# Optimization experiments

Hardware: AMD Instinct MI355X
Metric: run time of the kernel (lower is better)

## Reference

```python
import jax, jax.numpy as jnp
import numpy as np
from jax import lax


def conv2d(x, w, b=None, stride=1, pad=0):
    y = lax.conv_general_dilated(x, w, (stride, stride), [(pad, pad), (pad, pad)],
                                 dimension_numbers=('NCHW', 'OIHW', 'NCHW'))
    if b is not None:
        y = y + b[None, :, None, None]
    return y


def bilinear_resize_ac(S, Ho, Wo):
    # F.interpolate(..., mode='bilinear', align_corners=True)
    B, C, H, W = S.shape
    ys = jnp.linspace(0.0, H - 1.0, Ho)
    xs = jnp.linspace(0.0, W - 1.0, Wo)
    y0 = jnp.floor(ys).astype(jnp.int32); y1 = jnp.minimum(y0 + 1, H - 1); wy = ys - y0
    x0 = jnp.floor(xs).astype(jnp.int32); x1 = jnp.minimum(x0 + 1, W - 1); wx = xs - x0
    Sy = S[:, :, y0, :] * (1 - wy)[None, None, :, None] + S[:, :, y1, :] * wy[None, None, :, None]
    return Sy[:, :, :, x0] * (1 - wx)[None, None, None, :] + Sy[:, :, :, x1] * wx[None, None, None, :]


def deform_conv(x, offset, weight, bias=None, mask=None, stride=1, pad=1, dil=1):
    # (Modulated) deformable conv, deformable_groups=1; DCNv2 semantics:
    # offset channels are (dy, dx) pairs per kernel tap; zero padding outside.
    B, C, H, W = x.shape
    O, Ci, kh, kw = weight.shape
    K = kh * kw
    Ho, Wo = offset.shape[2], offset.shape[3]
    off = offset.reshape(B, K, 2, Ho, Wo)
    kyy, kxx = jnp.meshgrid(jnp.arange(kh) * dil, jnp.arange(kw) * dil, indexing='ij')
    kyy = kyy.reshape(K).astype(x.dtype); kxx = kxx.reshape(K).astype(x.dtype)
    base_y = (jnp.arange(Ho) * stride - pad).astype(x.dtype)
    base_x = (jnp.arange(Wo) * stride - pad).astype(x.dtype)
    py = base_y[None, None, :, None] + kyy[None, :, None, None] + off[:, :, 0]  # [B,K,Ho,Wo]
    px = base_x[None, None, None, :] + kxx[None, :, None, None] + off[:, :, 1]
    y0 = jnp.floor(py); x0 = jnp.floor(px)
    dy = py - y0; dx = px - x0
    y0i = y0.astype(jnp.int32); x0i = x0.astype(jnp.int32)
    xf = x.reshape(B, C, H * W)

    def corner(yi, xi, w):
        valid = (yi >= 0) & (yi <= H - 1) & (xi >= 0) & (xi <= W - 1)
        yc = jnp.clip(yi, 0, H - 1); xc = jnp.clip(xi, 0, W - 1)
        idx = (yc * W + xc).reshape(B, -1)  # [B, K*Ho*Wo]
        g = jax.vmap(lambda f, i: f[:, i])(xf, idx)  # [B, C, K*Ho*Wo]
        g = g.reshape(B, C, K, Ho, Wo)
        return g * (w * valid.astype(x.dtype))[:, None]

    s = (corner(y0i, x0i, (1 - dy) * (1 - dx))
         + corner(y0i, x0i + 1, (1 - dy) * dx)
         + corner(y0i + 1, x0i, dy * (1 - dx))
         + corner(y0i + 1, x0i + 1, dy * dx))  # [B,C,K,Ho,Wo]
    if mask is not None:
        s = s * mask[:, None]  # [B,1,K,Ho,Wo]
    out = jnp.einsum('bckhw,ock->bohw', s, weight.reshape(O, Ci, K))
    if bias is not None:
        out = out + bias[None, :, None, None]
    return out


def setup_inputs():
    key = jax.random.key(0)
    ks = jax.random.split(key, 16)
    B, Cin, Cout, H, W = 8, 256, 256, 64, 64

    def n(k, shape, s):
        return jax.random.normal(k, shape, jnp.float32) * s

    return {
        'x': jax.random.normal(ks[0], (B, Cin, H, W), jnp.float32),
        'S': jax.random.normal(ks[1], (B, 3, 128, 128), jnp.float32),
        'sp_w1': n(ks[2], (64, 3, 3, 3), 0.2), 'sp_b1': jnp.zeros(64), 'sp_s1': jnp.ones(64) + n(ks[3], (64,), 0.05), 'sp_o1': n(ks[3], (64,), 0.05),
        'sp_w2': n(ks[4], (64, 64, 3, 3), 0.05), 'sp_b2': jnp.zeros(64), 'sp_s2': jnp.ones(64) + n(ks[5], (64,), 0.05), 'sp_o2': n(ks[5], (64,), 0.05),
        'sp_w3': n(ks[6], (64, 64, 3, 3), 0.05), 'sp_b3': jnp.zeros(64), 'sp_s3': jnp.ones(64) + n(ks[7], (64,), 0.05), 'sp_o3': n(ks[7], (64,), 0.05),
        'off_w': n(ks[8], (18, 64, 3, 3), 0.05), 'off_b': jnp.zeros(18),
        'dc_off_w': n(ks[9], (18, 64, 3, 3), 0.05), 'dc_off_b': jnp.zeros(18),
        'dc_w': n(ks[10], (64, 64, 3, 3), 0.04),
        'm_w': n(ks[11], (9, 64, 1, 1), 0.1), 'm_b': jnp.zeros(9),
        'weight': n(ks[12], (Cout, Cin, 3, 3), 0.02), 'bias': jnp.zeros(Cout),
    }


def reference(x, S, sp_w1, sp_b1, sp_s1, sp_o1, sp_w2, sp_b2, sp_s2, sp_o2,
              sp_w3, sp_b3, sp_s3, sp_o3, off_w, off_b, dc_off_w, dc_off_b,
              dc_w, m_w, m_b, weight, bias):
    H, W = x.shape[2], x.shape[3]
    Si = bilinear_resize_ac(S, H, W)
    h = jax.nn.relu(conv2d(Si, sp_w1, sp_b1, 1, 1) * sp_s1[None, :, None, None] + sp_o1[None, :, None, None])
    h = jax.nn.relu(conv2d(h, sp_w2, sp_b2, 1, 1) * sp_s2[None, :, None, None] + sp_o2[None, :, None, None])
    h = jax.nn.relu(conv2d(h, sp_w3, sp_b3, 1, 1) * sp_s3[None, :, None, None] + sp_o3[None, :, None, None])
    offset = conv2d(h, off_w, off_b, 1, 1)                 # [B,18,H,W]
    dc_off = conv2d(h, dc_off_w, dc_off_b, 1, 1)           # internal offsets of weight_generator1 (DCNv1)
    feat = deform_conv(h, dc_off, dc_w, None, None, 1, 1, 1)
    mask = jax.nn.sigmoid(conv2d(feat, m_w, m_b, 1, 0))    # [B,9,H,W]
    return deform_conv(x, offset, weight, bias, mask, 1, 1, 1)
```

## Files before the change

kernel.cpp:

```cpp
#include <hip/hip_runtime.h>
#include <hip/hip_bf16.h>

typedef unsigned short u16;
typedef unsigned int u32;
typedef __attribute__((ext_vector_type(8))) short short8;
typedef __attribute__((ext_vector_type(4))) unsigned short ush4;
typedef __attribute__((ext_vector_type(16))) float f32x16;

#define OXT   0
#define OSI   (OXT + 8388608)
#define OA    (OSI + 98304)
#define OB    (OA + 2097152)
#define OC    (OB + 2097152)
#define OOFFS (OC + 2097152)
#define OMSK  (OOFFS + 1179648)
#define OWT   (OMSK + 294912)
#define OWSP1 (OWT + 589824)
#define OBSP1 (OWSP1 + 1728)
#define OWSP2 (OBSP1 + 64)
#define OBSP2 (OWSP2 + 36864)
#define OWSP3 (OBSP2 + 64)
#define OBSP3 (OWSP3 + 36864)
#define OWOFF (OBSP3 + 64)
#define OBOFF (OWOFF + 36864)
#define OWDC  (OBOFF + 64)

__device__ __forceinline__ u16 f2bf(float f) {
    __hip_bfloat16 hb = __float2bfloat16(f);
    return __builtin_bit_cast(u16, hb);
}
__device__ __forceinline__ float bf2f(u16 v) {
    return __builtin_bit_cast(float, (u32)v << 16);
}
__device__ __forceinline__ int sswz(int kg, int px) {
    return (px & ~7) | ((px ^ kg) & 7);
}

__global__ __launch_bounds__(256) void prep_k(
    const float* __restrict__ weight,
    const float* __restrict__ sp_w1, const float* __restrict__ sp_s1,
    const float* __restrict__ sp_w2, const float* __restrict__ sp_s2,
    const float* __restrict__ sp_w3, const float* __restrict__ sp_s3,
    const float* __restrict__ off_w, const float* __restrict__ dc_off_w,
    const float* __restrict__ dc_w,
    const float* __restrict__ sp_b1, const float* __restrict__ sp_o1,
    const float* __restrict__ sp_b2, const float* __restrict__ sp_o2,
    const float* __restrict__ sp_b3, const float* __restrict__ sp_o3,
    const float* __restrict__ off_b, const float* __restrict__ dc_off_b,
    float* __restrict__ ws)
{
    int i = blockIdx.x * 256 + threadIdx.x;
    if (i < 589824) {
        int j = i & 7; int o = (i >> 3) & 255; int kg = i >> 11;
        int K = kg * 8 + j; int k = K >> 8; int c = K & 255;
        ((u16*)(ws + OWT))[i] = f2bf(weight[o * 2304 + c * 9 + k]);
        return;
    }
    i -= 589824;
    if (i < 1728) {
        int o = i & 63; int kc = i >> 6; int c = kc % 3; int k = kc / 3;
        ws[OWSP1 + i] = sp_w1[(o * 3 + c) * 9 + k] * sp_s1[o];
        return;
    }
    i -= 1728;
    if (i < 36864) {
        int e = i & 7; int o = (i >> 3) & 63; int kg = (i >> 9) & 7; int tp = i >> 12;
        ((u16*)(ws + OWSP2))[i] = f2bf(sp_w2[(o * 64 + kg * 8 + e) * 9 + tp] * sp_s2[o]);
        return;
    }
    i -= 36864;
    if (i < 36864) {
        int e = i & 7; int o = (i >> 3) & 63; int kg = (i >> 9) & 7; int tp = i >> 12;
        ((u16*)(ws + OWSP3))[i] = f2bf(sp_w3[(o * 64 + kg * 8 + e) * 9 + tp] * sp_s3[o]);
        return;
    }
    i -= 36864;
    if (i < 36864) {
        int e = i & 7; int o = (i >> 3) & 63; int kg = (i >> 9) & 7; int tp = i >> 12;
        int c = kg * 8 + e;
        float v = 0.f;
        if (o < 18) v = off_w[(o * 64 + c) * 9 + tp];
        else if (o < 36) v = dc_off_w[((o - 18) * 64 + c) * 9 + tp];
        ((u16*)(ws + OWOFF))[i] = f2bf(v);
        return;
    }
    i -= 36864;
    if (i < 36864) {
        int e = i & 7; int o = (i >> 3) & 63; int kg = (i >> 9) & 7; int tp = i >> 12;
        ((u16*)(ws + OWDC))[i] = f2bf(dc_w[(o * 64 + kg * 8 + e) * 9 + tp]);
        return;
    }
    i -= 36864;
    if (i < 64) { ws[OBSP1 + i] = sp_b1[i] * sp_s1[i] + sp_o1[i]; return; }
    i -= 64;
    if (i < 64) { ws[OBSP2 + i] = sp_b2[i] * sp_s2[i] + sp_o2[i]; return; }
    i -= 64;
    if (i < 64) { ws[OBSP3 + i] = sp_b3[i] * sp_s3[i] + sp_o3[i]; return; }
    i -= 64;
    if (i < 64) { ws[OBOFF + i] = (i < 18) ? off_b[i] : (i < 36 ? dc_off_b[i - 18] : 0.f); return; }
}

__global__ __launch_bounds__(256) void transpose_x_k(const float* __restrict__ x,
                                                     u16* __restrict__ xT)
{
    __shared__ float tile[64][65];
    int blk = blockIdx.x;
    int chunk = blk & 3; int by = blk >> 2;
    int b = by >> 6; int y = by & 63;
    int c0 = chunk * 64;
    int t = threadIdx.x;
    for (int i = t; i < 4096; i += 256) {
        int ci = i >> 6, xi = i & 63;
        tile[ci][xi] = x[((b * 256 + c0 + ci) * 64 + y) * 64 + xi];
    }
    __syncthreads();
    for (int i = t; i < 4096; i += 256) {
        int xi = i >> 6, ci = i & 63;
        xT[((b * 64 + y) * 64 + xi) * 256 + c0 + ci] = f2bf(tile[ci][xi]);
    }
}

__global__ __launch_bounds__(256) void resize_k(const float* __restrict__ S,
                                                float* __restrict__ Si)
{
    int i = blockIdx.x * 256 + threadIdx.x;
    if (i >= 8 * 64 * 64 * 3) return;
    int c = i % 3; int x = (i / 3) & 63; int y = (i / 192) & 63; int b = i / 12288;
    const float sc = 127.0f / 63.0f;
    float sy = y * sc, sx = x * sc;
    float fy = floorf(sy), fx = floorf(sx);
    int y0 = (int)fy, x0 = (int)fx;
    int y1 = min(y0 + 1, 127), x1 = min(x0 + 1, 127);
    float wy = sy - fy, wx = sx - fx;
    const float* Sb = S + (size_t)(b * 3 + c) * 16384;
    float v00 = Sb[y0 * 128 + x0], v01 = Sb[y0 * 128 + x1];
    float v10 = Sb[y1 * 128 + x0], v11 = Sb[y1 * 128 + x1];
    Si[i] = (v00 * (1.f - wy) + v10 * wy) * (1.f - wx)
          + (v01 * (1.f - wy) + v11 * wy) * wx;
}

__global__ __launch_bounds__(256) void conv_in_k(const float* __restrict__ in,
                                                 const float* __restrict__ wt,
                                                 const float* __restrict__ bias,
                                                 u16* __restrict__ out)
{
    __shared__ float rows[3][66][3];
    int by = blockIdx.x; int b = by >> 6; int y = by & 63;
    int t = threadIdx.x;
    for (int i = t; i < 3 * 66 * 3; i += 256) {
        int r = i / 198; int rem = i - r * 198;
        int xi = rem / 3; int c = rem - xi * 3;
        int yy = y - 1 + r, xx = xi - 1;
        float v = 0.f;
        if (yy >= 0 && yy < 64 && xx >= 0 && xx < 64)
            v = in[(((b * 64 + yy) * 64 + xx) * 3) + c];
        rows[r][xi][c] = v;
    }
    __syncthreads();
    int o4 = (t & 15) * 4; int xg = t >> 4;
    float acc[4][4];
    #pragma unroll
    for (int oi = 0; oi < 4; oi++) {
        float bv = bias[o4 + oi];
        #pragma unroll
        for (int xi = 0; xi < 4; xi++) acc[oi][xi] = bv;
    }
    for (int k = 0; k < 9; k++) {
        int dy = k / 3, dx = k - 3 * (k / 3);
        for (int c = 0; c < 3; c++) {
            float4 w = *reinterpret_cast<const float4*>(&wt[(k * 3 + c) * 64 + o4]);
            #pragma unroll
            for (int xi = 0; xi < 4; xi++) {
                float iv = rows[dy][xg * 4 + xi + dx][c];
                acc[0][xi] = fmaf(w.x, iv, acc[0][xi]);
                acc[1][xi] = fmaf(w.y, iv, acc[1][xi]);
                acc[2][xi] = fmaf(w.z, iv, acc[2][xi]);
                acc[3][xi] = fmaf(w.w, iv, acc[3][xi]);
            }
        }
    }
    #pragma unroll
    for (int xi = 0; xi < 4; xi++) {
        int x = xg * 4 + xi;
        ush4 v;
        v.x = f2bf(fmaxf(acc[0][xi], 0.f));
        v.y = f2bf(fmaxf(acc[1][xi], 0.f));
        v.z = f2bf(fmaxf(acc[2][xi], 0.f));
        v.w = f2bf(fmaxf(acc[3][xi], 0.f));
        *reinterpret_cast<ush4*>(&out[((size_t)(by * 64 + x)) * 64 + o4]) = v;
    }
}

template <int MODE, bool RELU>
__global__ __launch_bounds__(256) void conv_mfma_k(const u16* __restrict__ in,
                                                   const u16* __restrict__ wm,
                                                   const float* __restrict__ bias,
                                                   u16* __restrict__ outH,
                                                   float* __restrict__ outF)
{
    __shared__ __attribute__((aligned(16))) char lds_h[3 * 66 * 128];
    __shared__ __attribute__((aligned(16))) u16 wtap[2][8][64][8];

    int t = threadIdx.x;
    int b = blockIdx.x >> 6; int y = blockIdx.x & 63;
    int pix0 = b * 4096 + y * 64;
    int wid = t >> 6, lane = t & 63;
    int lrow = lane & 31, lhi = lane >> 5;
    int o0 = (wid & 1) << 5;
    int px0 = (wid >> 1) << 5;
    int px = px0 + lrow;

    for (int i = t; i < 3 * 66 * 8; i += 256) {
        int r = i / 528; int rem = i - r * 528;
        int xi = rem >> 3; int g = rem & 7;
        int yy = y - 1 + r, xx = xi - 1;
        short8 v = {0,0,0,0,0,0,0,0};
        if (yy >= 0 && yy < 64 && xx >= 0 && xx < 64)
            v = *reinterpret_cast<const short8*>(&in[(size_t)((b * 4096 + yy * 64 + xx)) * 64 + g * 8]);
        int byte = (r * 66 + xi) * 128 + ((g * 16) ^ ((xi & 7) << 4));
        *reinterpret_cast<short8*>(lds_h + byte) = v;
    }
    {
        const char* gb = (const char*)(wm);
        char* lb = (char*)&wtap[0][0][0][0];
        #pragma unroll
        for (int i = 0; i < 2; i++) {
            int off = i * 4096 + wid * 1024;
            __builtin_amdgcn_global_load_lds(
                (const __attribute__((address_space(1))) void*)(gb + off + lane * 16),
                (__attribute__((address_space(3))) void*)(lb + off), 16, 0, 0);
        }
    }
    __syncthreads();

    f32x16 acc;
    #pragma unroll
    for (int r = 0; r < 16; r++) acc[r] = 0.f;

    #pragma unroll
    for (int tap = 0; tap < 9; tap++) {
        int cur = tap & 1, nxt = cur ^ 1;
        if (tap < 8) {
            const char* gb = (const char*)(wm + (size_t)(tap + 1) * 4096);
            char* lb = (char*)&wtap[nxt][0][0][0];
            #pragma unroll
            for (int i = 0; i < 2; i++) {
                int off = i * 4096 + wid * 1024;
                __builtin_amdgcn_global_load_lds(
                    (const __attribute__((address_space(1))) void*)(gb + off + lane * 16),
                    (__attribute__((address_space(3))) void*)(lb + off), 16, 0, 0);
            }
        }
        int dy = tap / 3, dx = tap - 3 * (tap / 3);
        int xi = px + dx;
        int rowbyte = (dy * 66 + xi) * 128;
        int swz = (xi & 7) << 4;
        #pragma unroll
        for (int ks = 0; ks < 4; ks++) {
            int kg = ks * 2 + lhi;
            short8 a0 = *reinterpret_cast<const short8*>(&wtap[cur][kg][o0 + lrow][0]);
            short8 b0 = *reinterpret_cast<const short8*>(lds_h + rowbyte + ((kg * 16) ^ swz));
            acc = __builtin_amdgcn_mfma_f32_32x32x16_bf16(a0, b0, acc, 0, 0, 0);
        }
        if (tap < 8) asm volatile("s_waitcnt vmcnt(0)" ::: "memory");
        __builtin_amdgcn_s_barrier();
    }
    __syncthreads();

    if (MODE == 0) {
        #pragma unroll
        for (int q = 0; q < 4; q++) {
            int ob = o0 + q * 8 + 4 * lhi;
            #pragma unroll
            for (int h = 0; h < 2; h++) {
                float v0 = acc[q * 4 + h * 2] + bias[ob + h * 2];
                float v1 = acc[q * 4 + h * 2 + 1] + bias[ob + h * 2 + 1];
                if (RELU) { v0 = fmaxf(v0, 0.f); v1 = fmaxf(v1, 0.f); }
                u32 pk = (u32)f2bf(v0) | ((u32)f2bf(v1) << 16);
                int byte = px * 128 + (((ob + h * 2) * 2) ^ ((px & 7) << 4));
                *reinterpret_cast<u32*>(lds_h + byte) = pk;
            }
        }
        __syncthreads();
        #pragma unroll
        for (int i = 0; i < 2; i++) {
            int cid = i * 256 + t;
            int p = cid >> 3, g = cid & 7;
            short8 v = *reinterpret_cast<const short8*>(lds_h + p * 128 + ((g * 16) ^ ((p & 7) << 4)));
            *reinterpret_cast<short8*>(&outH[(size_t)(pix0 + p) * 64 + g * 8]) = v;
        }
    } else {
        float* ltf = (float*)lds_h;
        #pragma unroll
        for (int r = 0; r < 16; r++) {
            int o = o0 + (r & 3) + ((r >> 2) << 3) + (lhi << 2);
            if (o < 36) ltf[px * 40 + o] = acc[r] + bias[o];
        }
        __syncthreads();
        for (int i = t; i < 576; i += 256) {
            int p = i / 9, q = i - 9 * (i / 9);
            float4 v = *reinterpret_cast<const float4*>(&ltf[p * 40 + q * 4]);
            *reinterpret_cast<float4*>(&outF[(size_t)(pix0 + p) * 36 + q * 4]) = v;
        }
    }
}

__global__ __launch_bounds__(512) void dconv_small_mfma(
    const u16* __restrict__ h, const float* __restrict__ offs,
    const u16* __restrict__ wdc, const float* __restrict__ m_w,
    const float* __restrict__ m_b, float* __restrict__ maskb)
{
    __shared__ __attribute__((aligned(16))) char smem[49152];
    u16 (*wtile)[8][64][8]  = (u16 (*)[8][64][8])smem;
    u16 (*stile)[8][128][8] = (u16 (*)[8][128][8])(smem + 16384);

    int t = threadIdx.x;
    int id = blockIdx.x;
    int blk = (id & 7) * 32 + (id >> 3);
    int pix0 = blk * 128;
    int b = pix0 >> 12;
    int wid = t >> 6, lane = t & 63;
    int lrow = lane & 31, lhi = lane >> 5;
    int o0 = (wid & 1) << 5;
    int px0 = (wid >> 1) << 5;
    int gp = t >> 2, gsub = t & 3;

    {
        const char* gb = (const char*)wdc;
        char* lb = (char*)&wtile[0][0][0][0];
        __builtin_amdgcn_global_load_lds(
            (const __attribute__((address_space(1))) void*)(gb + wid * 1024 + lane * 16),
            (__attribute__((address_space(3))) void*)(lb + wid * 1024), 16, 0, 0);
    }

    f32x16 acc;
    #pragma unroll
    for (int r = 0; r < 16; r++) acc[r] = 0.f;

    int car[4]; float cwr[4];

    for (int tap = 0; tap < 9; ++tap) {
        int cur = tap & 1, nxt = cur ^ 1;
        {
            int pix = pix0 + gp; int pib = pix & 4095;
            int y = pib >> 6, x = pib & 63;
            float offy = offs[(size_t)pix * 36 + 18 + tap * 2];
            float offx = offs[(size_t)pix * 36 + 18 + tap * 2 + 1];
            float py = (float)(y - 1 + tap / 3) + offy;
            float pxf = (float)(x - 1 + (tap % 3)) + offx;
            float fy = floorf(py), fx = floorf(pxf);
            int y0 = (int)fy, x0 = (int)fx;
            float dyf = py - fy, dxf = pxf - fx;
            #pragma unroll
            for (int j = 0; j < 4; j++) {
                float wj = ((j >> 1) ? dyf : 1.f - dyf) * ((j & 1) ? dxf : 1.f - dxf);
                int yy = y0 + (j >> 1), xx = x0 + (j & 1);
                bool valid = (yy >= 0 && yy < 64 && xx >= 0 && xx < 64);
                int yc = min(max(yy, 0), 63), xc = min(max(xx, 0), 63);
                car[j] = (b * 4096 + yc * 64 + xc) << 6;
                cwr[j] = valid ? wj : 0.f;
            }
        }
        int c = gsub << 4;
        float va[16];
        #pragma unroll
        for (int e = 0; e < 16; e++) va[e] = 0.f;
        #pragma unroll
        for (int j = 0; j < 4; j++) {
            float w = cwr[j];
            const u16* p = h + car[j] + c;
            short8 r0 = *reinterpret_cast<const short8*>(p);
            short8 r1 = *reinterpret_cast<const short8*>(p + 8);
            #pragma unroll
            for (int e = 0; e < 8; e++) {
                va[e]     = fmaf(w, bf2f((u16)r0[e]), va[e]);
                va[8 + e] = fmaf(w, bf2f((u16)r1[e]), va[8 + e]);
            }
        }
        short8 s0, s1;
        #pragma unroll
        for (int e = 0; e < 8; e++) { s0[e] = (short)f2bf(va[e]); s1[e] = (short)f2bf(va[8 + e]); }
        int kg0 = gsub * 2, kg1 = gsub * 2 + 1;
        *reinterpret_cast<short8*>(&stile[cur][kg0][sswz(kg0, gp)][0]) = s0;
        *reinterpret_cast<short8*>(&stile[cur][kg1][sswz(kg1, gp)][0]) = s1;

        asm volatile("s_waitcnt vmcnt(0) lgkmcnt(0)" ::: "memory");
        __builtin_amdgcn_s_barrier();

        #pragma unroll
        for (int ks = 0; ks < 4; ks++) {
            int kg = ks * 2 + lhi;
            short8 a0 = *reinterpret_cast<const short8*>(&wtile[cur][kg][o0 + lrow][0]);
            short8 b0 = *reinterpret_cast<const short8*>(&stile[cur][kg][sswz(kg, px0 + lrow)][0]);
            acc = __builtin_amdgcn_mfma_f32_32x32x16_bf16(a0, b0, acc, 0, 0, 0);
        }
        if (tap < 8) {
            const char* gb = (const char*)(wdc + (size_t)(tap + 1) * 4096);
            char* lb = (char*)&wtile[nxt][0][0][0];
            __builtin_amdgcn_global_load_lds(
                (const __attribute__((address_space(1))) void*)(gb + wid * 1024 + lane * 16),
                (__attribute__((address_space(3))) void*)(lb + wid * 1024), 16, 0, 0);
        }
    }

    __syncthreads();
    float* featl = (float*)smem;
    int pxl = px0 + lrow;
    #pragma unroll
    for (int r = 0; r < 16; r++) {
        int o = o0 + (r & 3) + ((r >> 2) << 3) + (lhi << 2);
        featl[pxl * 65 + o] = acc[r];
    }
    __syncthreads();
    if (t < 256) {
        int p = t >> 1, hh = t & 1;
        int pix = pix0 + p;
        const float* fr = &featl[p * 65];
        int j0 = hh ? 4 : 0, j1 = hh ? 9 : 4;
        for (int j = j0; j < j1; j++) {
            float a = m_b[j];
            #pragma unroll 8
            for (int cc = 0; cc < 64; cc++) a = fmaf(fr[cc], m_w[j * 64 + cc], a);
            maskb[(size_t)pix * 9 + j] = 1.f / (1.f + expf(-a));
        }
    }
}

__global__ __launch_bounds__(512) void dconv_big_mfma(
    const u16* __restrict__ xT, const float* __restrict__ offs,
    const float* __restrict__ maskb, const u16* __restrict__ wKg,
    const float* __restrict__ bias, float* __restrict__ out)
{
    __shared__ __attribute__((aligned(16))) u16 wtile[2][8][256][8];
    __shared__ __attribute__((aligned(16))) u16 stile[2][8][64][8];

    int t = threadIdx.x;
    int id = blockIdx.x;
    int blk = (id & 7) * 64 + (id >> 3);
    int pix0 = blk * 64;
    int b = pix0 >> 12, pib0 = pix0 & 4095;
    int wid = t >> 6, lane = t & 63;
    int lrow = lane & 31, lhi = lane >> 5;
    int o0 = wid << 5;
    int gp = t >> 3, gsub = t & 7;

    {
        const char* gb = (const char*)wKg;
        char* lb = (char*)&wtile[0][0][0][0];
        #pragma unroll
        for (int i = 0; i < 4; i++) {
            int off = i * 8192 + wid * 1024;
            __builtin_amdgcn_global_load_lds(
                (const __attribute__((address_space(1))) void*)(gb + off + lane * 16),
                (__attribute__((address_space(3))) void*)(lb + off), 16, 0, 0);
        }
    }

    f32x16 acc[2];
    #pragma unroll
    for (int fp = 0; fp < 2; fp++)
        #pragma unroll
        for (int r = 0; r < 16; r++) acc[fp][r] = 0.f;

    int car[4]; float cwr[4];

    for (int kt = 0; kt < 36; ++kt) {
        int cur = kt & 1, nxt = cur ^ 1;
        int tap = kt >> 2, chunk = kt & 3;

        if (chunk == 0) {
            int pix = pix0 + gp; int pib = pix & 4095;
            int y = pib >> 6, x = pib & 63;
            float offy = offs[(size_t)pix * 36 + tap * 2];
            float offx = offs[(size_t)pix * 36 + tap * 2 + 1];
            float m = maskb[(size_t)pix * 9 + tap];
            float py = (float)(y - 1 + tap / 3) + offy;
            float pxf = (float)(x - 1 + (tap % 3)) + offx;
            float fy = floorf(py), fx = floorf(pxf);
            int y0 = (int)fy, x0 = (int)fx;
            float dyf = py - fy, dxf = pxf - fx;
            #pragma unroll
            for (int j = 0; j < 4; j++) {
                float wj = ((j >> 1) ? dyf : 1.f - dyf) * ((j & 1) ? dxf : 1.f - dxf);
                int yy = y0 + (j >> 1), xx = x0 + (j & 1);
                bool valid = (yy >= 0 && yy < 64 && xx >= 0 && xx < 64);
                int yc = min(max(yy, 0), 63), xc = min(max(xx, 0), 63);
                car[j] = (b * 4096 + yc * 64 + xc) << 8;
                cwr[j] = valid ? wj * m : 0.f;
            }
        }

        int c = (chunk << 6) + (gsub << 3);
        float va[8];
        #pragma unroll
        for (int e = 0; e < 8; e++) va[e] = 0.f;
        #pragma unroll
        for (int j = 0; j < 4; j++) {
            float w = cwr[j];
            short8 r0 = *reinterpret_cast<const short8*>(xT + car[j] + c);
            #pragma unroll
            for (int e = 0; e < 8; e++) va[e] = fmaf(w, bf2f((u16)r0[e]), va[e]);
        }
        short8 s0;
        #pragma unroll
        for (int e = 0; e < 8; e++) s0[e] = (short)f2bf(va[e]);
        *reinterpret_cast<short8*>(&stile[cur][gsub][sswz(gsub, gp)][0]) = s0;

        asm volatile("s_waitcnt vmcnt(0) lgkmcnt(0)" ::: "memory");
        __builtin_amdgcn_s_barrier();

        #pragma unroll
        for (int ks = 0; ks < 4; ks++) {
            int kg = ks * 2 + lhi;
            short8 a0 = *reinterpret_cast<const short8*>(&wtile[cur][kg][o0 + lrow][0]);
            short8 b0 = *reinterpret_cast<const short8*>(&stile[cur][kg][sswz(kg, lrow)][0]);
            short8 b1 = *reinterpret_cast<const short8*>(&stile[cur][kg][sswz(kg, 32 + lrow)][0]);
            acc[0] = __builtin_amdgcn_mfma_f32_32x32x16_bf16(a0, b0, acc[0], 0, 0, 0);
            acc[1] = __builtin_amdgcn_mfma_f32_32x32x16_bf16(a0, b1, acc[1], 0, 0, 0);
        }
        if (kt < 35) {
            const char* gb = (const char*)(wKg + (size_t)(kt + 1) * 16384);
            char* lb = (char*)&wtile[nxt][0][0][0];
            #pragma unroll
            for (int i = 0; i < 4; i++) {
                int off = i * 8192 + wid * 1024;
                __builtin_amdgcn_global_load_lds(
                    (const __attribute__((address_space(1))) void*)(gb + off + lane * 16),
                    (__attribute__((address_space(3))) void*)(lb + off), 16, 0, 0);
            }
        }
    }

    #pragma unroll
    for (int fp = 0; fp < 2; fp++) {
        #pragma unroll
        for (int r = 0; r < 16; r++) {
            int o = o0 + (r & 3) + ((r >> 2) << 3) + (lhi << 2);
            size_t rowoff = ((size_t)(b * 256 + o) << 12) + pib0;
            out[rowoff + fp * 32 + lrow] = acc[fp][r] + bias[o];
        }
    }
}

extern "C" void kernel_launch(void* const* d_in, const int* in_sizes, int n_in,
                              void* d_out, int out_size, void* d_ws, size_t ws_size,
                              hipStream_t stream)
{
    const float* x        = (const float*)d_in[0];
    const float* S        = (const float*)d_in[1];
    const float* sp_w1    = (const float*)d_in[2];
    const float* sp_b1    = (const float*)d_in[3];
    const float* sp_s1    = (const float*)d_in[4];
    const float* sp_o1    = (const float*)d_in[5];
    const float* sp_w2    = (const float*)d_in[6];
    const float* sp_b2    = (const float*)d_in[7];
    const float* sp_s2    = (const float*)d_in[8];
    const float* sp_o2    = (const float*)d_in[9];
    const float* sp_w3    = (const float*)d_in[10];
    const float* sp_b3    = (const float*)d_in[11];
    const float* sp_s3    = (const float*)d_in[12];
    const float* sp_o3    = (const float*)d_in[13];
    const float* off_w    = (const float*)d_in[14];
    const float* off_b    = (const float*)d_in[15];
    const float* dc_off_w = (const float*)d_in[16];
    const float* dc_off_b = (const float*)d_in[17];
    const float* dc_w     = (const float*)d_in[18];
    const float* m_w      = (const float*)d_in[19];
    const float* m_b      = (const float*)d_in[20];
    const float* weight   = (const float*)d_in[21];
    const float* bias     = (const float*)d_in[22];
    float* out = (float*)d_out;
    float* ws  = (float*)d_ws;

    u16*   xTb   = (u16*)(ws + OXT);
    float* Si    = ws + OSI;
    u16*   h1    = (u16*)(ws + OA);
    u16*   h2    = (u16*)(ws + OB);
    u16*   h3    = (u16*)(ws + OC);
    float* offsb = ws + OOFFS;
    float* maskb = ws + OMSK;

    prep_k<<<2888, 256, 0, stream>>>(weight, sp_w1, sp_s1, sp_w2, sp_s2, sp_w3, sp_s3,
                                     off_w, dc_off_w, dc_w,
                                     sp_b1, sp_o1, sp_b2, sp_o2, sp_b3, sp_o3,
                                     off_b, dc_off_b, ws);
    transpose_x_k<<<2048, 256, 0, stream>>>(x, xTb);
    resize_k<<<384, 256, 0, stream>>>(S, Si);
    conv_in_k<<<512, 256, 0, stream>>>(Si, ws + OWSP1, ws + OBSP1, h1);
    conv_mfma_k<0, true><<<512, 256, 0, stream>>>(h1, (const u16*)(ws + OWSP2),
                                                  ws + OBSP2, h2, nullptr);
    conv_mfma_k<0, true><<<512, 256, 0, stream>>>(h2, (const u16*)(ws + OWSP3),
                                                  ws + OBSP3, h3, nullptr);
    conv_mfma_k<1, false><<<512, 256, 0, stream>>>(h3, (const u16*)(ws + OWOFF),
                                                   ws + OBOFF, nullptr, offsb);
    dconv_small_mfma<<<256, 512, 0, stream>>>(h3, offsb, (const u16*)(ws + OWDC),
                                              m_w, m_b, maskb);
    dconv_big_mfma<<<512, 512, 0, stream>>>(xTb, offsb, maskb,
                                            (const u16*)(ws + OWT), bias, out);
}
```

Before: 147.5 us.

## Enlarge dconv_big pixel tile to 128 and prefetch bilinear gathers one step ahead

The final deformable conv kernel now handles 128 pixels per block instead of 64. Each wave computes a 64x64 output tile with four MFMA accumulators, so every weight tile streamed through LDS is reused across twice as many pixels, and the grid shrinks from 512 to 256 blocks. The corner gathers from xT for the next K-chunk are issued into registers before the barrier and waited with a partial vmcnt, so gather latency overlaps the current MFMA work. The cost is higher register pressure (8 short8 prefetch registers plus 64 accumulator floats), twice the stile LDS, and half as many blocks, which may underfill the 256 CUs.

```diff
diff --git a/kernel.cpp b/kernel.cpp
--- a/kernel.cpp
+++ b/kernel.cpp
@@ -36,6 +36,32 @@
     return (px & ~7) | ((px ^ kg) & 7);
 }
 
+__device__ __forceinline__ void corner_tab_big(
+    int tap, int pix0, int b, int gp,
+    const float* __restrict__ offs, const float* __restrict__ maskb,
+    int* car, float* cwr)
+{
+    int pix = pix0 + gp; int pib = pix & 4095;
+    int y = pib >> 6, x = pib & 63;
+    float offy = offs[(size_t)pix * 36 + tap * 2];
+    float offx = offs[(size_t)pix * 36 + tap * 2 + 1];
+    float m = maskb[(size_t)pix * 9 + tap];
+    float py = (float)(y - 1 + tap / 3) + offy;
+    float pxf = (float)(x - 1 + (tap % 3)) + offx;
+    float fy = floorf(py), fx = floorf(pxf);
+    int y0 = (int)fy, x0 = (int)fx;
+    float dyf = py - fy, dxf = pxf - fx;
+    #pragma unroll
+    for (int j = 0; j < 4; j++) {
+        float wj = ((j >> 1) ? dyf : 1.f - dyf) * ((j & 1) ? dxf : 1.f - dxf);
+        int yy = y0 + (j >> 1), xx = x0 + (j & 1);
+        bool valid = (yy >= 0 && yy < 64 && xx >= 0 && xx < 64);
+        int yc = min(max(yy, 0), 63), xc = min(max(xx, 0), 63);
+        car[j] = (b * 4096 + yc * 64 + xc) << 8;
+        cwr[j] = valid ? wj * m : 0.f;
+    }
+}
+
 __global__ __launch_bounds__(256) void prep_k(
     const float* __restrict__ weight,
     const float* __restrict__ sp_w1, const float* __restrict__ sp_s1,
@@ -432,18 +458,32 @@
     const float* __restrict__ bias, float* __restrict__ out)
 {
     __shared__ __attribute__((aligned(16))) u16 wtile[2][8][256][8];
-    __shared__ __attribute__((aligned(16))) u16 stile[2][8][64][8];
+    __shared__ __attribute__((aligned(16))) u16 stile[2][8][128][8];
 
     int t = threadIdx.x;
     int id = blockIdx.x;
-    int blk = (id & 7) * 64 + (id >> 3);
-    int pix0 = blk * 64;
+    int blk = (id & 7) * 32 + (id >> 3);
+    int pix0 = blk * 128;
     int b = pix0 >> 12, pib0 = pix0 & 4095;
     int wid = t >> 6, lane = t & 63;
     int lrow = lane & 31, lhi = lane >> 5;
-    int o0 = wid << 5;
-    int gp = t >> 3, gsub = t & 7;
-
+    int o0 = (wid & 3) << 6;
+    int px0 = (wid >> 2) << 6;
+    int gp = t >> 2, gsub = t & 3;
+
+    int car[4]; float cwr[4];
+    short8 g[8];
+
+    corner_tab_big(0, pix0, b, gp, offs, maskb, car, cwr);
+    {
+        int c = gsub << 4;
+        #pragma unroll
+        for (int j = 0; j < 4; j++) {
+            const u16* p = xT + car[j] + c;
+            g[j * 2]     = *reinterpret_cast<const short8*>(p);
+            g[j * 2 + 1] = *reinterpret_cast<const short8*>(p + 8);
+        }
+    }
     {
         const char* gb = (const char*)wKg;
         char* lb = (char*)&wtile[0][0][0][0];
@@ -456,67 +496,63 @@
         }
     }
 
-    f32x16 acc[2];
-    #pragma unroll
-    for (int fp = 0; fp < 2; fp++)
-        #pragma unroll
-        for (int r = 0; r < 16; r++) acc[fp][r] = 0.f;
-
-    int car[4]; float cwr[4];
+    f32x16 acc[2][2];
+    #pragma unroll
+    for (int ao = 0; ao < 2; ao++)
+        #pragma unroll
+        for (int bp = 0; bp < 2; bp++)
+            #pragma unroll
+            for (int r = 0; r < 16; r++) acc[ao][bp][r] = 0.f;
 
     for (int kt = 0; kt < 36; ++kt) {
         int cur = kt & 1, nxt = cur ^ 1;
-        int tap = kt >> 2, chunk = kt & 3;
-
-        if (chunk == 0) {
-            int pix = pix0 + gp; int pib = pix & 4095;
-            int y = pib >> 6, x = pib & 63;
-            float offy = offs[(size_t)pix * 36 + tap * 2];
-            float offx = offs[(size_t)pix * 36 + tap * 2 + 1];
-            float m = maskb[(size_t)pix * 9 + tap];
-            float py = (float)(y - 1 + tap / 3) + offy;
-            float pxf = (float)(x - 1 + (tap % 3)) + offx;
-            float fy = floorf(py), fx = floorf(pxf);
-            int y0 = (int)fy, x0 = (int)fx;
-            float dyf = py - fy, dxf = pxf - fx;
-            #pragma unroll
-            for (int j = 0; j < 4; j++) {
-                float wj = ((j >> 1) ? dyf : 1.f - dyf) * ((j & 1) ? dxf : 1.f - dxf);
-                int yy = y0 + (j >> 1), xx = x0 + (j & 1);
-                bool valid = (yy >= 0 && yy < 64 && xx >= 0 && xx < 64);
-                int yc = min(max(yy, 0), 63), xc = min(max(xx, 0), 63);
-                car[j] = (b * 4096 + yc * 64 + xc) << 8;
-                cwr[j] = valid ? wj * m : 0.f;
-            }
-        }
-
-        int c = (chunk << 6) + (gsub << 3);
-        float va[8];
-        #pragma unroll
-        for (int e = 0; e < 8; e++) va[e] = 0.f;
+
+        float va[16];
+        #pragma unroll
+        for (int e = 0; e < 16; e++) va[e] = 0.f;
         #pragma unroll
         for (int j = 0; j < 4; j++) {
             float w = cwr[j];
-            short8 r0 = *reinterpret_cast<const short8*>(xT + car[j] + c);
-            #pragma unroll
-            for (int e = 0; e < 8; e++) va[e] = fmaf(w, bf2f((u16)r0[e]), va[e]);
-        }
-        short8 s0;
-        #pragma unroll
-        for (int e = 0; e < 8; e++) s0[e] = (short)f2bf(va[e]);
-        *reinterpret_cast<short8*>(&stile[cur][gsub][sswz(gsub, gp)][0]) = s0;
-
-        asm volatile("s_waitcnt vmcnt(0) lgkmcnt(0)" ::: "memory");
+            #pragma unroll
+            for (int e = 0; e < 8; e++) {
+                va[e]     = fmaf(w, bf2f((u16)g[j * 2][e]), va[e]);
+                va[8 + e] = fmaf(w, bf2f((u16)g[j * 2 + 1][e]), va[8 + e]);
+            }
+        }
+        short8 s0, s1;
+        #pragma unroll
+        for (int e = 0; e < 8; e++) { s0[e] = (short)f2bf(va[e]); s1[e] = (short)f2bf(va[8 + e]); }
+        int kg0 = gsub * 2, kg1 = gsub * 2 + 1;
+        *reinterpret_cast<short8*>(&stile[cur][kg0][sswz(kg0, gp)][0]) = s0;
+        *reinterpret_cast<short8*>(&stile[cur][kg1][sswz(kg1, gp)][0]) = s1;
+
+        if (kt < 35) {
+            if (((kt + 1) & 3) == 0)
+                corner_tab_big((kt + 1) >> 2, pix0, b, gp, offs, maskb, car, cwr);
+            int c = (((kt + 1) & 3) << 6) + (gsub << 4);
+            #pragma unroll
+            for (int j = 0; j < 4; j++) {
+                const u16* p = xT + car[j] + c;
+                g[j * 2]     = *reinterpret_cast<const short8*>(p);
+                g[j * 2 + 1] = *reinterpret_cast<const short8*>(p + 8);
+            }
+            asm volatile("s_waitcnt vmcnt(8) lgkmcnt(0)" ::: "memory");
+        } else {
+            asm volatile("s_waitcnt vmcnt(0) lgkmcnt(0)" ::: "memory");
+        }
         __builtin_amdgcn_s_barrier();
 
         #pragma unroll
         for (int ks = 0; ks < 4; ks++) {
             int kg = ks * 2 + lhi;
             short8 a0 = *reinterpret_cast<const short8*>(&wtile[cur][kg][o0 + lrow][0]);
-            short8 b0 = *reinterpret_cast<const short8*>(&stile[cur][kg][sswz(kg, lrow)][0]);
-            short8 b1 = *reinterpret_cast<const short8*>(&stile[cur][kg][sswz(kg, 32 + lrow)][0]);
-            acc[0] = __builtin_amdgcn_mfma_f32_32x32x16_bf16(a0, b0, acc[0], 0, 0, 0);
-            acc[1] = __builtin_amdgcn_mfma_f32_32x32x16_bf16(a0, b1, acc[1], 0, 0, 0);
+            short8 a1 = *reinterpret_cast<const short8*>(&wtile[cur][kg][o0 + 32 + lrow][0]);
+            short8 b0 = *reinterpret_cast<const short8*>(&stile[cur][kg][sswz(kg, px0 + lrow)][0]);
+            short8 b1 = *reinterpret_cast<const short8*>(&stile[cur][kg][sswz(kg, px0 + 32 + lrow)][0]);
+            acc[0][0] = __builtin_amdgcn_mfma_f32_32x32x16_bf16(a0, b0, acc[0][0], 0, 0, 0);
+            acc[0][1] = __builtin_amdgcn_mfma_f32_32x32x16_bf16(a0, b1, acc[0][1], 0, 0, 0);
+            acc[1][0] = __builtin_amdgcn_mfma_f32_32x32x16_bf16(a1, b0, acc[1][0], 0, 0, 0);
+            acc[1][1] = __builtin_amdgcn_mfma_f32_32x32x16_bf16(a1, b1, acc[1][1], 0, 0, 0);
         }
         if (kt < 35) {
             const char* gb = (const char*)(wKg + (size_t)(kt + 1) * 16384);
@@ -532,12 +568,14 @@
     }
 
     #pragma unroll
-    for (int fp = 0; fp < 2; fp++) {
+    for (int ao = 0; ao < 2; ao++) {
         #pragma unroll
         for (int r = 0; r < 16; r++) {
-            int o = o0 + (r & 3) + ((r >> 2) << 3) + (lhi << 2);
-            size_t rowoff = ((size_t)(b * 256 + o) << 12) + pib0;
-            out[rowoff + fp * 32 + lrow] = acc[fp][r] + bias[o];
+            int o = o0 + ao * 32 + (r & 3) + ((r >> 2) << 3) + (lhi << 2);
+            float bv = bias[o];
+            size_t rowoff = ((size_t)(b * 256 + o) << 12) + pib0 + px0;
+            out[rowoff + lrow] = acc[ao][0][r] + bv;
+            out[rowoff + 32 + lrow] = acc[ao][1][r] + bv;
         }
     }
 }
@@ -595,6 +633,6 @@
                                                    ws + OBOFF, nullptr, offsb);
     dconv_small_mfma<<<256, 512, 0, stream>>>(h3, offsb, (const u16*)(ws + OWDC),
                                               m_w, m_b, maskb);
-    dconv_big_mfma<<<512, 512, 0, stream>>>(xTb, offsb, maskb,
+    dconv_big_mfma<<<256, 512, 0, stream>>>(xTb, offsb, maskb,
                                             (const u16*)(ws + OWT), bias, out);
 }
```

Result: faster. 137.1 us (-7.1%).

## Software-pipeline deform gather and load weights directly into registers

Applied to the files above, without the earlier changes.

The big deformable conv kernel drops the LDS weight tile and has each wave load its MFMA A fragments straight from global memory into registers. The wave-to-tile mapping changes to 64 output channels by 32 pixels. The bilinear gather for the next K-chunk is issued one iteration ahead, so its global loads overlap the current MFMAs, and the barrier only waits on LDS. This aims to hide gather latency and cut LDS traffic and vmcnt stalls, at the cost of more registers (launch bounds 512,4) and repeated weight reads from L2.

```diff
diff --git a/kernel.cpp b/kernel.cpp
--- a/kernel.cpp
+++ b/kernel.cpp
@@ -34,6 +34,32 @@
 }
 __device__ __forceinline__ int sswz(int kg, int px) {
     return (px & ~7) | ((px ^ kg) & 7);
+}
+
+__device__ __forceinline__ void corner_tab_big(
+    int tap, int pix0, int b, int gp,
+    const float* __restrict__ offs, const float* __restrict__ maskb,
+    int* car, float* cwr)
+{
+    int pix = pix0 + gp; int pib = pix & 4095;
+    int y = pib >> 6, x = pib & 63;
+    float offy = offs[(size_t)pix * 36 + tap * 2];
+    float offx = offs[(size_t)pix * 36 + tap * 2 + 1];
+    float m = maskb[(size_t)pix * 9 + tap];
+    float py = (float)(y - 1 + tap / 3) + offy;
+    float pxf = (float)(x - 1 + (tap % 3)) + offx;
+    float fy = floorf(py), fx = floorf(pxf);
+    int y0 = (int)fy, x0 = (int)fx;
+    float dyf = py - fy, dxf = pxf - fx;
+    #pragma unroll
+    for (int j = 0; j < 4; j++) {
+        float wj = ((j >> 1) ? dyf : 1.f - dyf) * ((j & 1) ? dxf : 1.f - dxf);
+        int yy = y0 + (j >> 1), xx = x0 + (j & 1);
+        bool valid = (yy >= 0 && yy < 64 && xx >= 0 && xx < 64);
+        int yc = min(max(yy, 0), 63), xc = min(max(xx, 0), 63);
+        car[j] = (b * 4096 + yc * 64 + xc) << 8;
+        cwr[j] = valid ? wj * m : 0.f;
+    }
 }
 
 __global__ __launch_bounds__(256) void prep_k(
@@ -426,12 +452,11 @@
     }
 }
 
-__global__ __launch_bounds__(512) void dconv_big_mfma(
+__global__ __launch_bounds__(512, 4) void dconv_big_mfma(
     const u16* __restrict__ xT, const float* __restrict__ offs,
     const float* __restrict__ maskb, const u16* __restrict__ wKg,
     const float* __restrict__ bias, float* __restrict__ out)
 {
-    __shared__ __attribute__((aligned(16))) u16 wtile[2][8][256][8];
     __shared__ __attribute__((aligned(16))) u16 stile[2][8][64][8];
 
     int t = threadIdx.x;
@@ -441,103 +466,114 @@
     int b = pix0 >> 12, pib0 = pix0 & 4095;
     int wid = t >> 6, lane = t & 63;
     int lrow = lane & 31, lhi = lane >> 5;
-    int o0 = wid << 5;
+    int o0 = (wid & 3) << 6;
+    int px0 = (wid >> 2) << 5;
     int gp = t >> 3, gsub = t & 7;
 
+    int car[4]; float cwr[4];
+    short8 g[4];
+    short8 a[8];
+
+    corner_tab_big(0, pix0, b, gp, offs, maskb, car, cwr);
     {
-        const char* gb = (const char*)wKg;
-        char* lb = (char*)&wtile[0][0][0][0];
-        #pragma unroll
-        for (int i = 0; i < 4; i++) {
-            int off = i * 8192 + wid * 1024;
-            __builtin_amdgcn_global_load_lds(
-                (const __attribute__((address_space(1))) void*)(gb + off + lane * 16),
-                (__attribute__((address_space(3))) void*)(lb + off), 16, 0, 0);
-        }
-    }
+        int c = gsub << 3;
+        #pragma unroll
+        for (int j = 0; j < 4; j++)
+            g[j] = *reinterpret_cast<const short8*>(xT + car[j] + c);
+    }
+    {
+        #pragma unroll
+        for (int ks = 0; ks < 4; ks++) {
+            int kgg = ks * 2 + lhi;
+            const u16* base = wKg + ((size_t)kgg * 256 + o0 + lrow) * 8;
+            a[ks]     = *reinterpret_cast<const short8*>(base);
+            a[4 + ks] = *reinterpret_cast<const short8*>(base + 256);
+        }
+    }
+    {
+        float va[8];
+        #pragma unroll
+        for (int e = 0; e < 8; e++) va[e] = 0.f;
+        #pragma unroll
+        for (int j = 0; j < 4; j++) {
+            float w = cwr[j];
+            #pragma unroll
+            for (int e = 0; e < 8; e++) va[e] = fmaf(w, bf2f((u16)g[j][e]), va[e]);
+        }
+        short8 s0;
+        #pragma unroll
+        for (int e = 0; e < 8; e++) s0[e] = (short)f2bf(va[e]);
+        *reinterpret_cast<short8*>(&stile[0][gsub][sswz(gsub, gp)][0]) = s0;
+    }
+    {
+        int c = 64 + (gsub << 3);
+        #pragma unroll
+        for (int j = 0; j < 4; j++)
+            g[j] = *reinterpret_cast<const short8*>(xT + car[j] + c);
+    }
+    asm volatile("s_waitcnt lgkmcnt(0)" ::: "memory");
+    __builtin_amdgcn_s_barrier();
 
     f32x16 acc[2];
     #pragma unroll
-    for (int fp = 0; fp < 2; fp++)
-        #pragma unroll
-        for (int r = 0; r < 16; r++) acc[fp][r] = 0.f;
-
-    int car[4]; float cwr[4];
+    for (int ao = 0; ao < 2; ao++)
+        #pragma unroll
+        for (int r = 0; r < 16; r++) acc[ao][r] = 0.f;
 
     for (int kt = 0; kt < 36; ++kt) {
         int cur = kt & 1, nxt = cur ^ 1;
-        int tap = kt >> 2, chunk = kt & 3;
-
-        if (chunk == 0) {
-            int pix = pix0 + gp; int pib = pix & 4095;
-            int y = pib >> 6, x = pib & 63;
-            float offy = offs[(size_t)pix * 36 + tap * 2];
-            float offx = offs[(size_t)pix * 36 + tap * 2 + 1];
-            float m = maskb[(size_t)pix * 9 + tap];
-            float py = (float)(y - 1 + tap / 3) + offy;
-            float pxf = (float)(x - 1 + (tap % 3)) + offx;
-            float fy = floorf(py), fx = floorf(pxf);
-            int y0 = (int)fy, x0 = (int)fx;
-            float dyf = py - fy, dxf = pxf - fx;
-            #pragma unroll
-            for (int j = 0; j < 4; j++) {
-                float wj = ((j >> 1) ? dyf : 1.f - dyf) * ((j & 1) ? dxf : 1.f - dxf);
-                int yy = y0 + (j >> 1), xx = x0 + (j & 1);
-                bool valid = (yy >= 0 && yy < 64 && xx >= 0 && xx < 64);
-                int yc = min(max(yy, 0), 63), xc = min(max(xx, 0), 63);
-                car[j] = (b * 4096 + yc * 64 + xc) << 8;
-                cwr[j] = valid ? wj * m : 0.f;
-            }
-        }
-
-        int c = (chunk << 6) + (gsub << 3);
-        float va[8];
-        #pragma unroll
-        for (int e = 0; e < 8; e++) va[e] = 0.f;
-        #pragma unroll
-        for (int j = 0; j < 4; j++) {
-            float w = cwr[j];
-            short8 r0 = *reinterpret_cast<const short8*>(xT + car[j] + c);
-            #pragma unroll
-            for (int e = 0; e < 8; e++) va[e] = fmaf(w, bf2f((u16)r0[e]), va[e]);
-        }
-        short8 s0;
-        #pragma unroll
-        for (int e = 0; e < 8; e++) s0[e] = (short)f2bf(va[e]);
-        *reinterpret_cast<short8*>(&stile[cur][gsub][sswz(gsub, gp)][0]) = s0;
-
-        asm volatile("s_waitcnt vmcnt(0) lgkmcnt(0)" ::: "memory");
-        __builtin_amdgcn_s_barrier();
 
         #pragma unroll
         for (int ks = 0; ks < 4; ks++) {
             int kg = ks * 2 + lhi;
-            short8 a0 = *reinterpret_cast<const short8*>(&wtile[cur][kg][o0 + lrow][0]);
-            short8 b0 = *reinterpret_cast<const short8*>(&stile[cur][kg][sswz(kg, lrow)][0]);
-            short8 b1 = *reinterpret_cast<const short8*>(&stile[cur][kg][sswz(kg, 32 + lrow)][0]);
-            acc[0] = __builtin_amdgcn_mfma_f32_32x32x16_bf16(a0, b0, acc[0], 0, 0, 0);
-            acc[1] = __builtin_amdgcn_mfma_f32_32x32x16_bf16(a0, b1, acc[1], 0, 0, 0);
-        }
+            short8 bf = *reinterpret_cast<const short8*>(&stile[cur][kg][sswz(kg, px0 + lrow)][0]);
+            acc[0] = __builtin_amdgcn_mfma_f32_32x32x16_bf16(a[ks], bf, acc[0], 0, 0, 0);
+            acc[1] = __builtin_amdgcn_mfma_f32_32x32x16_bf16(a[4 + ks], bf, acc[1], 0, 0, 0);
+        }
+
         if (kt < 35) {
-            const char* gb = (const char*)(wKg + (size_t)(kt + 1) * 16384);
-            char* lb = (char*)&wtile[nxt][0][0][0];
             #pragma unroll
-            for (int i = 0; i < 4; i++) {
-                int off = i * 8192 + wid * 1024;
-                __builtin_amdgcn_global_load_lds(
-                    (const __attribute__((address_space(1))) void*)(gb + off + lane * 16),
-                    (__attribute__((address_space(3))) void*)(lb + off), 16, 0, 0);
-            }
-        }
-    }
-
-    #pragma unroll
-    for (int fp = 0; fp < 2; fp++) {
+            for (int ks = 0; ks < 4; ks++) {
+                int kgg = (kt + 1) * 8 + ks * 2 + lhi;
+                const u16* base = wKg + ((size_t)kgg * 256 + o0 + lrow) * 8;
+                a[ks]     = *reinterpret_cast<const short8*>(base);
+                a[4 + ks] = *reinterpret_cast<const short8*>(base + 256);
+            }
+            {
+                float va[8];
+                #pragma unroll
+                for (int e = 0; e < 8; e++) va[e] = 0.f;
+                #pragma unroll
+                for (int j = 0; j < 4; j++) {
+                    float w = cwr[j];
+                    #pragma unroll
+                    for (int e = 0; e < 8; e++) va[e] = fmaf(w, bf2f((u16)g[j][e]), va[e]);
+                }
+                short8 s0;
+                #pragma unroll
+                for (int e = 0; e < 8; e++) s0[e] = (short)f2bf(va[e]);
+                *reinterpret_cast<short8*>(&stile[nxt][gsub][sswz(gsub, gp)][0]) = s0;
+            }
+            if (kt < 34) {
+                if (((kt + 2) & 3) == 0)
+                    corner_tab_big((kt + 2) >> 2, pix0, b, gp, offs, maskb, car, cwr);
+                int c = (((kt + 2) & 3) << 6) + (gsub << 3);
+                #pragma unroll
+                for (int j = 0; j < 4; j++)
+                    g[j] = *reinterpret_cast<const short8*>(xT + car[j] + c);
+            }
+            asm volatile("s_waitcnt lgkmcnt(0)" ::: "memory");
+            __builtin_amdgcn_s_barrier();
+        }
+    }
+
+    #pragma unroll
+    for (int ao = 0; ao < 2; ao++) {
         #pragma unroll
         for (int r = 0; r < 16; r++) {
-            int o = o0 + (r & 3) + ((r >> 2) << 3) + (lhi << 2);
-            size_t rowoff = ((size_t)(b * 256 + o) << 12) + pib0;
-            out[rowoff + fp * 32 + lrow] = acc[fp][r] + bias[o];
+            int o = o0 + ao * 32 + (r & 3) + ((r >> 2) << 3) + (lhi << 2);
+            size_t rowoff = ((size_t)(b * 256 + o) << 12) + pib0 + px0;
+            out[rowoff + lrow] = acc[ao][r] + bias[o];
         }
     }
 }
```

New measurement: 147.8 us. No clear change (+0.2%).
